# Kernel optimization log

Measured on AMD Instinct MI355X. Metric: run time of the kernel, lower is better.

## Reference

```python
import jax, jax.numpy as jnp
import numpy as np

EMBED_DIM = 1024
NUM_HEADS = 16
RANK = 32
HEAD_DIM = EMBED_DIM // NUM_HEADS
SCALE = 1.0 / np.sqrt(RANK).astype(np.float32)


def setup_inputs() -> dict:
    key = jax.random.key(0)
    ks = jax.random.split(key, 9)
    B, S = 2, 2048
    def lin(k, fan_in, fan_out):
        bound = 1.0 / np.sqrt(fan_in)
        return jax.random.uniform(k, (fan_in, fan_out), jnp.float32, -bound, bound)
    return {
        "hidden_states": jax.random.normal(ks[0], (B, S, EMBED_DIM), jnp.float32),
        "Wq": lin(ks[1], EMBED_DIM, RANK * NUM_HEADS),
        "bq": jnp.zeros((RANK * NUM_HEADS,), jnp.float32),
        "Wk": lin(ks[2], EMBED_DIM, RANK * NUM_HEADS),
        "bk": jnp.zeros((RANK * NUM_HEADS,), jnp.float32),
        "Wv": lin(ks[3], EMBED_DIM, EMBED_DIM),
        "bv": jnp.zeros((EMBED_DIM,), jnp.float32),
        "Wo": lin(ks[4], EMBED_DIM, EMBED_DIM),
        "bo": jnp.zeros((EMBED_DIM,), jnp.float32),
    }


def reference(hidden_states, Wq, bq, Wk, bk, Wv, bv, Wo, bo):
    B, S, E = hidden_states.shape
    q = (hidden_states @ Wq + bq).reshape(B, S, NUM_HEADS, RANK)      # [b,i,h,r]
    k = (hidden_states @ Wk + bk).reshape(B, S, NUM_HEADS, RANK)      # [b,j,h,r]
    v = (hidden_states @ Wv + bv).reshape(B, S, NUM_HEADS, HEAD_DIM)  # [b,j,h,d]
    # full [b,i,j,h] score tensor, softmax over j (axis=2), as in the torch code
    scores = jnp.einsum('bihr,bjhr->bijh', q, k) * SCALE
    attn = jax.nn.softmax(scores, axis=2)
    out = jnp.einsum('bijh,bjhd->bihd', attn, v).reshape(B, S, E)
    return out @ Wo + bo
```

## Files before the change

### kernel.cpp

```cpp
#include <hip/hip_runtime.h>

#define EMBED   1024
#define NHEADS  16
#define RANK    32
#define HDIM    64
#define BATCH   2
#define SEQ     2048
#define BSQ     (BATCH * SEQ)
#define CEXP    0.25505998f

typedef __attribute__((ext_vector_type(8))) short bf16x8;
typedef __attribute__((ext_vector_type(4))) float f32x4;

__device__ __forceinline__ float bf2f(unsigned short u) {
    union { unsigned int i; float f; } x; x.i = ((unsigned int)u) << 16;
    return x.f;
}
__device__ __forceinline__ unsigned short f2bf(float f) {
    union { float f; unsigned int i; } x; x.f = f;
    unsigned int r = x.i + 0x7FFFu + ((x.i >> 16) & 1u);
    return (unsigned short)(r >> 16);
}

#define ASYNC16(gp, lp) \
    __builtin_amdgcn_global_load_lds( \
        (const __attribute__((address_space(1))) void*)(gp), \
        (__attribute__((address_space(3))) void*)(lp), 16, 0, 0)

__global__ __launch_bounds__(256) void prep_all(
    const float* __restrict__ hs,
    const float* __restrict__ Wq, const float* __restrict__ Wk,
    const float* __restrict__ Wv, const float* __restrict__ Wo,
    const float* __restrict__ bq, const float* __restrict__ bk,
    const float* __restrict__ bv,
    unsigned short* __restrict__ hsb, unsigned short* __restrict__ wT_all,
    unsigned short* __restrict__ woT, float* __restrict__ ball)
{
    __shared__ float L[64][65];
    const int blk = blockIdx.x;
    const int t = threadIdx.x;

    if (blk < 2048) {
        const size_t i = ((size_t)blk * 256 + t) * 8;
        float4 v0 = *(const float4*)(hs + i);
        float4 v1 = *(const float4*)(hs + i + 4);
        ushort4 o0, o1;
        o0.x = f2bf(v0.x); o0.y = f2bf(v0.y); o0.z = f2bf(v0.z); o0.w = f2bf(v0.w);
        o1.x = f2bf(v1.x); o1.y = f2bf(v1.y); o1.z = f2bf(v1.z); o1.w = f2bf(v1.w);
        *(ushort4*)(hsb + i) = o0;
        *(ushort4*)(hsb + i + 4) = o1;
        return;
    }
    if (blk < 2816) {
        int idx = blk - 2048;
        int z, bx, by;
        if (idx < 256) { z = idx >> 7; int r2 = idx & 127; bx = r2 & 7; by = r2 >> 3; }
        else { idx -= 256; z = 2 + (idx >> 8); int r2 = idx & 255; bx = r2 & 15; by = r2 >> 4; }
        const int Nw = (z < 2) ? 512 : 1024;
        const float* W = (z == 0) ? Wq : (z == 1) ? Wk : (z == 2) ? Wv : Wo;
        unsigned short* dst = (z == 3) ? woT : (wT_all + (size_t)z * 512 * 1024);

        const int r = t >> 2, c0 = (t & 3) * 16;
        const float* src = W + (size_t)(by * 64 + r) * Nw + bx * 64 + c0;
        #pragma unroll
        for (int u = 0; u < 4; u++)
            *(float4*)&L[r][c0 + 4 * u] = *(const float4*)(src + 4 * u);
        __syncthreads();
        unsigned short* drow = dst + (size_t)(bx * 64 + r) * 1024 + by * 64 + c0;
        #pragma unroll
        for (int u4 = 0; u4 < 4; u4++) {
            ushort4 o;
            o.x = f2bf(L[c0 + 4 * u4 + 0][r]);
            o.y = f2bf(L[c0 + 4 * u4 + 1][r]);
            o.z = f2bf(L[c0 + 4 * u4 + 2][r]);
            o.w = f2bf(L[c0 + 4 * u4 + 3][r]);
            *(ushort4*)(drow + 4 * u4) = o;
        }
        return;
    }
    {
        const int i = (blk - 2816) * 256 + t;
        ball[i] = (i < 512) ? bq[i] : (i < 1024) ? bk[i - 512] : bv[i - 1024];
    }
}

__global__ __launch_bounds__(256) void gemm_qkv(
    const unsigned short* __restrict__ A, const unsigned short* __restrict__ BT,
    const float* __restrict__ bias,
    unsigned short* __restrict__ qH, unsigned short* __restrict__ kH,
    unsigned short* __restrict__ vTout)
{
    __shared__ unsigned short As[2 * 128 * 32];
    __shared__ unsigned short Bs[2 * 128 * 32];
    const int K = 1024;
    const int t = threadIdx.x;
    const int lane = t & 63;
    const int li = lane & 15, la = lane >> 4;
    const int w = t >> 6, wm = w >> 1, wn = w & 1;
    const int row0 = blockIdx.y * 128, col0 = blockIdx.x * 128;

    const int sr = lane >> 2, sc2 = (lane & 3) * 8;
    const unsigned short* ag = A + (size_t)(row0 + sr) * K + sc2;
    const unsigned short* bg = BT + (size_t)(col0 + sr) * K + sc2;

    f32x4 acc[4][4];
    #pragma unroll
    for (int i = 0; i < 4; i++)
        #pragma unroll
        for (int j = 0; j < 4; j++)
            acc[i][j] = (f32x4){0.f, 0.f, 0.f, 0.f};

    for (int k0 = 0; k0 < K; k0 += 64) {
        #pragma unroll
        for (int kh = 0; kh < 2; kh++)
            #pragma unroll
            for (int u = 0; u < 2; u++) {
                const int ro = w * 32 + u * 16;
                ASYNC16(ag + (size_t)ro * K + k0 + kh * 32, &As[kh * 4096 + ro * 32]);
                ASYNC16(bg + (size_t)ro * K + k0 + kh * 32, &Bs[kh * 4096 + ro * 32]);
            }
        __syncthreads();
        #pragma unroll
        for (int kh = 0; kh < 2; kh++) {
            bf16x8 af[4], bfr[4];
            #pragma unroll
            for (int mt = 0; mt < 4; mt++)
                af[mt] = *(const bf16x8*)&As[kh * 4096 + (wm * 64 + mt * 16 + li) * 32 + la * 8];
            #pragma unroll
            for (int nt = 0; nt < 4; nt++)
                bfr[nt] = *(const bf16x8*)&Bs[kh * 4096 + (wn * 64 + nt * 16 + li) * 32 + la * 8];
            #pragma unroll
            for (int mt = 0; mt < 4; mt++)
                #pragma unroll
                for (int nt = 0; nt < 4; nt++)
                    acc[mt][nt] = __builtin_amdgcn_mfma_f32_16x16x32_bf16(af[mt], bfr[nt], acc[mt][nt], 0, 0, 0);
        }
        __syncthreads();
    }

    const int bb = row0 >> 11;
    const int jb = (row0 & 2047) + wm * 64;
    #pragma unroll
    for (int nt = 0; nt < 4; nt++) {
        const int col = col0 + wn * 64 + nt * 16 + li;
        const float bval = bias[col];
        if (col < 1024) {
            const int hh = (col & 511) >> 5;
            const int rr = col & 31;
            unsigned short* base = ((col < 512) ? qH : kH)
                + ((size_t)(bb * 16 + hh) * 2048) * 32 + rr;
            #pragma unroll
            for (int mt = 0; mt < 4; mt++)
                #pragma unroll
                for (int r = 0; r < 4; r++)
                    base[(size_t)(jb + mt * 16 + la * 4 + r) * 32] =
                        f2bf(acc[mt][nt][r] + bval);
        } else {
            const int hd = col - 1024;
            unsigned short* dcol = vTout + ((size_t)(bb * 16 + (hd >> 6)) * 64 + (hd & 63)) * SEQ;
            #pragma unroll
            for (int mt = 0; mt < 4; mt++) {
                const int srow = jb + mt * 16 + la * 4;
                ushort4 o;
                o.x = f2bf(acc[mt][nt][0] + bval);
                o.y = f2bf(acc[mt][nt][1] + bval);
                o.z = f2bf(acc[mt][nt][2] + bval);
                o.w = f2bf(acc[mt][nt][3] + bval);
                *(ushort4*)(dcol + srow) = o;
            }
        }
    }
}

__global__ __launch_bounds__(256) void gemm_out(
    const unsigned short* __restrict__ A, const unsigned short* __restrict__ BT,
    const float* __restrict__ bias, float* __restrict__ C)
{
    __shared__ unsigned short As[2 * 64 * 32];
    __shared__ unsigned short Bs[2 * 128 * 32];
    const int K = 1024;
    const int t = threadIdx.x;
    const int lane = t & 63;
    const int li = lane & 15, la = lane >> 4;
    const int w = t >> 6, wm = w >> 1, wn = w & 1;
    const int row0 = blockIdx.y * 64, col0 = blockIdx.x * 128;

    const int sr = lane >> 2, sc2 = (lane & 3) * 8;
    const unsigned short* ag = A + (size_t)(row0 + sr) * K + sc2;
    const unsigned short* bg = BT + (size_t)(col0 + sr) * K + sc2;

    f32x4 acc[2][4];
    #pragma unroll
    for (int i = 0; i < 2; i++)
        #pragma unroll
        for (int j = 0; j < 4; j++)
            acc[i][j] = (f32x4){0.f, 0.f, 0.f, 0.f};

    for (int k0 = 0; k0 < K; k0 += 64) {
        #pragma unroll
        for (int kh = 0; kh < 2; kh++) {
            ASYNC16(ag + (size_t)(w * 16) * K + k0 + kh * 32, &As[kh * 2048 + (w * 16) * 32]);
            #pragma unroll
            for (int u = 0; u < 2; u++) {
                const int ro = w * 32 + u * 16;
                ASYNC16(bg + (size_t)ro * K + k0 + kh * 32, &Bs[kh * 4096 + ro * 32]);
            }
        }
        __syncthreads();
        #pragma unroll
        for (int kh = 0; kh < 2; kh++) {
            bf16x8 af[2], bfr[4];
            #pragma unroll
            for (int mt = 0; mt < 2; mt++)
                af[mt] = *(const bf16x8*)&As[kh * 2048 + (wm * 32 + mt * 16 + li) * 32 + la * 8];
            #pragma unroll
            for (int nt = 0; nt < 4; nt++)
                bfr[nt] = *(const bf16x8*)&Bs[kh * 4096 + (wn * 64 + nt * 16 + li) * 32 + la * 8];
            #pragma unroll
            for (int mt = 0; mt < 2; mt++)
                #pragma unroll
                for (int nt = 0; nt < 4; nt++)
                    acc[mt][nt] = __builtin_amdgcn_mfma_f32_16x16x32_bf16(af[mt], bfr[nt], acc[mt][nt], 0, 0, 0);
        }
        __syncthreads();
    }

    #pragma unroll
    for (int nt = 0; nt < 4; nt++) {
        const int col = col0 + wn * 64 + nt * 16 + li;
        const float bval = bias[col];
        #pragma unroll
        for (int mt = 0; mt < 2; mt++)
            #pragma unroll
            for (int r = 0; r < 4; r++) {
                const int row = row0 + wm * 32 + mt * 16 + la * 4 + r;
                C[(size_t)row * 1024 + col] = acc[mt][nt][r] + bval;
            }
    }
}

__global__ __launch_bounds__(256) void attn_v8(
    const unsigned short* __restrict__ qH,
    const unsigned short* __restrict__ kH,
    const unsigned short* __restrict__ vT,
    unsigned short* __restrict__ ao)
{
    __shared__ unsigned short kt[2][64 * 48];
    __shared__ unsigned short vt[2][64 * 72];
    __shared__ unsigned short P[64 * 72];

    const int t = threadIdx.x;
    const int lane = t & 63;
    const int li = lane & 15, la = lane >> 4;
    const int w = t >> 6;

    const int bh = blockIdx.x & 31;
    const int itile = blockIdx.x >> 5;
    const int i0 = itile * 64;
    const int b = bh >> 4, h = bh & 15;

    bf16x8 qf;
    {
        const unsigned short* qp = qH + ((size_t)bh * 2048 + i0 + w * 16 + li) * 32 + la * 8;
        ushort4 q0 = *(const ushort4*)qp;
        ushort4 q1 = *(const ushort4*)(qp + 4);
        short u[8];
        u[0] = (short)f2bf(bf2f(q0.x) * CEXP);
        u[1] = (short)f2bf(bf2f(q0.y) * CEXP);
        u[2] = (short)f2bf(bf2f(q0.z) * CEXP);
        u[3] = (short)f2bf(bf2f(q0.w) * CEXP);
        u[4] = (short)f2bf(bf2f(q1.x) * CEXP);
        u[5] = (short)f2bf(bf2f(q1.y) * CEXP);
        u[6] = (short)f2bf(bf2f(q1.z) * CEXP);
        u[7] = (short)f2bf(bf2f(q1.w) * CEXP);
        qf = *(const bf16x8*)u;
    }

    bf16x8 vones;
    #pragma unroll
    for (int u2 = 0; u2 < 8; u2++) vones[u2] = (short)0x3F80;

    const int kr = t >> 2, kc = (t & 3) * 8;
    const int vr = t >> 3, vc = (t & 7) * 8;
    const unsigned short* kp = kH + (size_t)bh * 2048 * 32 + (size_t)kr * 32 + kc;
    const unsigned short* vp0 = vT + (size_t)bh * 64 * SEQ + (size_t)vr * SEQ + vc;
    const unsigned short* vp1 = vp0 + (size_t)32 * SEQ;

    f32x4 accO[4], accl;
    accl = (f32x4){0.f, 0.f, 0.f, 0.f};
    #pragma unroll
    for (int dt = 0; dt < 4; dt++) accO[dt] = (f32x4){0.f, 0.f, 0.f, 0.f};
    const int prow = w * 16 + li;

    uint4 kreg  = *(const uint4*)(kp);
    uint4 vreg0 = *(const uint4*)(vp0);
    uint4 vreg1 = *(const uint4*)(vp1);
    *(uint4*)&kt[0][kr * 48 + kc] = kreg;
    *(uint4*)&vt[0][vr * 72 + vc] = vreg0;
    *(uint4*)&vt[0][(vr + 32) * 72 + vc] = vreg1;
    kreg  = *(const uint4*)(kp + 64 * 32);
    vreg0 = *(const uint4*)(vp0 + 64);
    vreg1 = *(const uint4*)(vp1 + 64);

    #define ATTN_BODY(BUF, OTHER, JPRE)                                            \
    {                                                                              \
        __syncthreads();                                                           \
        *(uint4*)&kt[OTHER][kr * 48 + kc] = kreg;                                  \
        *(uint4*)&vt[OTHER][vr * 72 + vc] = vreg0;                                 \
        *(uint4*)&vt[OTHER][(vr + 32) * 72 + vc] = vreg1;                          \
        const int jn = (JPRE) & 2047;                                              \
        kreg  = *(const uint4*)(kp + (size_t)jn * 32);                             \
        vreg0 = *(const uint4*)(vp0 + jn);                                         \
        vreg1 = *(const uint4*)(vp1 + jn);                                         \
        f32x4 sc[4];                                                               \
        _Pragma("unroll")                                                          \
        for (int jt = 0; jt < 4; jt++) {                                           \
            const bf16x8 kf = *(const bf16x8*)&kt[BUF][(jt * 16 + li) * 48 + la * 8]; \
            sc[jt] = __builtin_amdgcn_mfma_f32_16x16x32_bf16(kf, qf, (f32x4){0.f,0.f,0.f,0.f}, 0, 0, 0); \
        }                                                                          \
        _Pragma("unroll")                                                          \
        for (int jt = 0; jt < 4; jt++) {                                           \
            union { float f; unsigned int u; } c0, c1, c2, c3;                     \
            c0.f = exp2f(sc[jt][0]);                                               \
            c1.f = exp2f(sc[jt][1]);                                               \
            c2.f = exp2f(sc[jt][2]);                                               \
            c3.f = exp2f(sc[jt][3]);                                               \
            uint2 pk;                                                              \
            pk.x = __builtin_amdgcn_perm(c1.u + 0x8000u, c0.u + 0x8000u, 0x07060302u); \
            pk.y = __builtin_amdgcn_perm(c3.u + 0x8000u, c2.u + 0x8000u, 0x07060302u); \
            *(uint2*)&P[prow * 72 + jt * 16 + la * 4] = pk;                        \
        }                                                                          \
        _Pragma("unroll")                                                          \
        for (int ks = 0; ks < 2; ks++) {                                           \
            const bf16x8 pf = *(const bf16x8*)&P[prow * 72 + ks * 32 + la * 8];    \
            accl = __builtin_amdgcn_mfma_f32_16x16x32_bf16(pf, vones, accl, 0, 0, 0); \
            _Pragma("unroll")                                                      \
            for (int dt = 0; dt < 4; dt++) {                                       \
                const bf16x8 vf = *(const bf16x8*)&vt[BUF][(dt * 16 + li) * 72 + ks * 32 + la * 8]; \
                accO[dt] = __builtin_amdgcn_mfma_f32_16x16x32_bf16(pf, vf, accO[dt], 0, 0, 0); \
            }                                                                      \
        }                                                                          \
    }

    for (int j0 = 0; j0 < SEQ; j0 += 128) {
        ATTN_BODY(0, 1, j0 + 128)
        ATTN_BODY(1, 0, j0 + 192)
    }
    #undef ATTN_BODY

    float linv[4];
    #pragma unroll
    for (int r = 0; r < 4; r++) linv[r] = 1.f / accl[r];
    #pragma unroll
    for (int dt = 0; dt < 4; dt++)
        #pragma unroll
        for (int r = 0; r < 4; r++) {
            const int row = b * SEQ + i0 + w * 16 + la * 4 + r;
            ao[(size_t)row * 1024 + h * 64 + dt * 16 + li] = f2bf(accO[dt][r] * linv[r]);
        }
}

extern "C" void kernel_launch(void* const* d_in, const int* in_sizes, int n_in,
                              void* d_out, int out_size, void* d_ws, size_t ws_size,
                              hipStream_t stream) {
    const float* hs = (const float*)d_in[0];
    const float* Wq = (const float*)d_in[1];
    const float* bq = (const float*)d_in[2];
    const float* Wk = (const float*)d_in[3];
    const float* bk = (const float*)d_in[4];
    const float* Wv = (const float*)d_in[5];
    const float* bv = (const float*)d_in[6];
    const float* Wo = (const float*)d_in[7];
    const float* bo = (const float*)d_in[8];

    char* p = (char*)d_ws;
    unsigned short* hsb = (unsigned short*)(p);
    unsigned short* wT  = (unsigned short*)(p + 8388608u);
    unsigned short* woT = (unsigned short*)(p + 12582912u);
    float*          ball= (float*)(p + 14680064u);
    unsigned short* qHb = (unsigned short*)(p + 14688256u);
    unsigned short* kHb = (unsigned short*)(p + 18882560u);
    unsigned short* vTb = (unsigned short*)(p + 23076864u);
    unsigned short* ao  = (unsigned short*)(p + 31465472u);

    prep_all<<<dim3(2824), 256, 0, stream>>>(hs, Wq, Wk, Wv, Wo, bq, bk, bv,
                                             hsb, wT, woT, ball);

    gemm_qkv<<<dim3(16, 32), 256, 0, stream>>>(hsb, wT, ball, qHb, kHb, vTb);

    attn_v8<<<dim3(1024), 256, 0, stream>>>(qHb, kHb, vTb, ao);

    gemm_out<<<dim3(8, 64), 256, 0, stream>>>(ao, woT, bo, (float*)d_out);
}
```

Measured before the change: 189.5 us.

## Double-buffer LDS tiles in QKV/out GEMMs and simplify attention prefetch addressing

The QKV and output projection GEMMs now use two LDS buffers, so the next K-tile is loaded asynchronously while MFMAs run on the current one. This is meant to hide global-load latency that the single-buffer version exposed before every compute step. The cost is double the shared memory per block, which may lower occupancy. The attention kernel's K/V prefetch now uses incrementing pointers instead of wrapped index math. That removes the wrap, so the final iterations read past the end of each head's slice; the data is never used, but the read may go past the buffer end for the last head.

Measured after the change: 196.4 us. +3.7%, slower.

```diff
diff --git a/kernel.cpp b/kernel.cpp
--- a/kernel.cpp
+++ b/kernel.cpp
@@ -90,8 +90,8 @@
     unsigned short* __restrict__ qH, unsigned short* __restrict__ kH,
     unsigned short* __restrict__ vTout)
 {
-    __shared__ unsigned short As[2 * 128 * 32];
-    __shared__ unsigned short Bs[2 * 128 * 32];
+    __shared__ unsigned short As[2][128 * 64];
+    __shared__ unsigned short Bs[2][128 * 64];
     const int K = 1024;
     const int t = threadIdx.x;
     const int lane = t & 63;
@@ -103,6 +103,18 @@
     const unsigned short* ag = A + (size_t)(row0 + sr) * K + sc2;
     const unsigned short* bg = BT + (size_t)(col0 + sr) * K + sc2;
 
+#define STAGE_QKV(BUF, KOFF)                                                     \
+    {                                                                            \
+        _Pragma("unroll")                                                        \
+        for (int kh = 0; kh < 2; kh++)                                           \
+            _Pragma("unroll")                                                    \
+            for (int u = 0; u < 2; u++) {                                        \
+                const int ro = w * 32 + u * 16;                                  \
+                ASYNC16(ag + (size_t)ro * K + (KOFF) + kh * 32, &As[BUF][kh * 4096 + ro * 32]); \
+                ASYNC16(bg + (size_t)ro * K + (KOFF) + kh * 32, &Bs[BUF][kh * 4096 + ro * 32]); \
+            }                                                                    \
+    }
+
     f32x4 acc[4][4];
     #pragma unroll
     for (int i = 0; i < 4; i++)
@@ -110,25 +122,21 @@
         for (int j = 0; j < 4; j++)
             acc[i][j] = (f32x4){0.f, 0.f, 0.f, 0.f};
 
+    STAGE_QKV(0, 0)
+    __syncthreads();
+
     for (int k0 = 0; k0 < K; k0 += 64) {
-        #pragma unroll
-        for (int kh = 0; kh < 2; kh++)
-            #pragma unroll
-            for (int u = 0; u < 2; u++) {
-                const int ro = w * 32 + u * 16;
-                ASYNC16(ag + (size_t)ro * K + k0 + kh * 32, &As[kh * 4096 + ro * 32]);
-                ASYNC16(bg + (size_t)ro * K + k0 + kh * 32, &Bs[kh * 4096 + ro * 32]);
-            }
-        __syncthreads();
+        const int cur = (k0 >> 6) & 1;
+        if (k0 + 64 < K) STAGE_QKV(cur ^ 1, k0 + 64)
         #pragma unroll
         for (int kh = 0; kh < 2; kh++) {
             bf16x8 af[4], bfr[4];
             #pragma unroll
             for (int mt = 0; mt < 4; mt++)
-                af[mt] = *(const bf16x8*)&As[kh * 4096 + (wm * 64 + mt * 16 + li) * 32 + la * 8];
+                af[mt] = *(const bf16x8*)&As[cur][kh * 4096 + (wm * 64 + mt * 16 + li) * 32 + la * 8];
             #pragma unroll
             for (int nt = 0; nt < 4; nt++)
-                bfr[nt] = *(const bf16x8*)&Bs[kh * 4096 + (wn * 64 + nt * 16 + li) * 32 + la * 8];
+                bfr[nt] = *(const bf16x8*)&Bs[cur][kh * 4096 + (wn * 64 + nt * 16 + li) * 32 + la * 8];
             #pragma unroll
             for (int mt = 0; mt < 4; mt++)
                 #pragma unroll
@@ -137,6 +145,7 @@
         }
         __syncthreads();
     }
+#undef STAGE_QKV
 
     const int bb = row0 >> 11;
     const int jb = (row0 & 2047) + wm * 64;
@@ -176,8 +185,8 @@
     const unsigned short* __restrict__ A, const unsigned short* __restrict__ BT,
     const float* __restrict__ bias, float* __restrict__ C)
 {
-    __shared__ unsigned short As[2 * 64 * 32];
-    __shared__ unsigned short Bs[2 * 128 * 32];
+    __shared__ unsigned short As[2][64 * 64];
+    __shared__ unsigned short Bs[2][128 * 64];
     const int K = 1024;
     const int t = threadIdx.x;
     const int lane = t & 63;
@@ -189,6 +198,19 @@
     const unsigned short* ag = A + (size_t)(row0 + sr) * K + sc2;
     const unsigned short* bg = BT + (size_t)(col0 + sr) * K + sc2;
 
+#define STAGE_OUT(BUF, KOFF)                                                     \
+    {                                                                            \
+        _Pragma("unroll")                                                        \
+        for (int kh = 0; kh < 2; kh++) {                                         \
+            ASYNC16(ag + (size_t)(w * 16) * K + (KOFF) + kh * 32, &As[BUF][kh * 2048 + (w * 16) * 32]); \
+            _Pragma("unroll")                                                    \
+            for (int u = 0; u < 2; u++) {                                        \
+                const int ro = w * 32 + u * 16;                                  \
+                ASYNC16(bg + (size_t)ro * K + (KOFF) + kh * 32, &Bs[BUF][kh * 4096 + ro * 32]); \
+            }                                                                    \
+        }                                                                        \
+    }
+
     f32x4 acc[2][4];
     #pragma unroll
     for (int i = 0; i < 2; i++)
@@ -196,26 +218,21 @@
         for (int j = 0; j < 4; j++)
             acc[i][j] = (f32x4){0.f, 0.f, 0.f, 0.f};
 
+    STAGE_OUT(0, 0)
+    __syncthreads();
+
     for (int k0 = 0; k0 < K; k0 += 64) {
-        #pragma unroll
-        for (int kh = 0; kh < 2; kh++) {
-            ASYNC16(ag + (size_t)(w * 16) * K + k0 + kh * 32, &As[kh * 2048 + (w * 16) * 32]);
-            #pragma unroll
-            for (int u = 0; u < 2; u++) {
-                const int ro = w * 32 + u * 16;
-                ASYNC16(bg + (size_t)ro * K + k0 + kh * 32, &Bs[kh * 4096 + ro * 32]);
-            }
-        }
-        __syncthreads();
+        const int cur = (k0 >> 6) & 1;
+        if (k0 + 64 < K) STAGE_OUT(cur ^ 1, k0 + 64)
         #pragma unroll
         for (int kh = 0; kh < 2; kh++) {
             bf16x8 af[2], bfr[4];
             #pragma unroll
             for (int mt = 0; mt < 2; mt++)
-                af[mt] = *(const bf16x8*)&As[kh * 2048 + (wm * 32 + mt * 16 + li) * 32 + la * 8];
+                af[mt] = *(const bf16x8*)&As[cur][kh * 2048 + (wm * 32 + mt * 16 + li) * 32 + la * 8];
             #pragma unroll
             for (int nt = 0; nt < 4; nt++)
-                bfr[nt] = *(const bf16x8*)&Bs[kh * 4096 + (wn * 64 + nt * 16 + li) * 32 + la * 8];
+                bfr[nt] = *(const bf16x8*)&Bs[cur][kh * 4096 + (wn * 64 + nt * 16 + li) * 32 + la * 8];
             #pragma unroll
             for (int mt = 0; mt < 2; mt++)
                 #pragma unroll
@@ -224,6 +241,7 @@
         }
         __syncthreads();
     }
+#undef STAGE_OUT
 
     #pragma unroll
     for (int nt = 0; nt < 4; nt++) {
@@ -301,17 +319,19 @@
     kreg  = *(const uint4*)(kp + 64 * 32);
     vreg0 = *(const uint4*)(vp0 + 64);
     vreg1 = *(const uint4*)(vp1 + 64);
-
-    #define ATTN_BODY(BUF, OTHER, JPRE)                                            \
+    const unsigned short* kpf  = kp + 2 * 64 * 32;
+    const unsigned short* vpf0 = vp0 + 128;
+    const unsigned short* vpf1 = vp1 + 128;
+
+    #define ATTN_BODY(BUF, OTHER, KOFF, VOFF)                                      \
     {                                                                              \
         __syncthreads();                                                           \
         *(uint4*)&kt[OTHER][kr * 48 + kc] = kreg;                                  \
         *(uint4*)&vt[OTHER][vr * 72 + vc] = vreg0;                                 \
         *(uint4*)&vt[OTHER][(vr + 32) * 72 + vc] = vreg1;                          \
-        const int jn = (JPRE) & 2047;                                              \
-        kreg  = *(const uint4*)(kp + (size_t)jn * 32);                             \
-        vreg0 = *(const uint4*)(vp0 + jn);                                         \
-        vreg1 = *(const uint4*)(vp1 + jn);                                         \
+        kreg  = *(const uint4*)(kpf + (KOFF));                                     \
+        vreg0 = *(const uint4*)(vpf0 + (VOFF));                                    \
+        vreg1 = *(const uint4*)(vpf1 + (VOFF));                                    \
         f32x4 sc[4];                                                               \
         _Pragma("unroll")                                                          \
         for (int jt = 0; jt < 4; jt++) {                                           \
@@ -343,8 +363,11 @@
     }
 
     for (int j0 = 0; j0 < SEQ; j0 += 128) {
-        ATTN_BODY(0, 1, j0 + 128)
-        ATTN_BODY(1, 0, j0 + 192)
+        ATTN_BODY(0, 1, 0, 0)
+        ATTN_BODY(1, 0, 64 * 32, 64)
+        kpf  += 128 * 32;
+        vpf0 += 128;
+        vpf1 += 128;
     }
     #undef ATTN_BODY
 
```

## Process 128 query rows per attention block to reuse K/V tiles

Applied to the files above, without the earlier changes.

Each attention block now covers 128 query rows instead of 64, and each wave handles two 16-row query tiles. Every K/V tile staged in shared memory therefore serves twice as many score and PV MFMAs, which halves global K/V traffic and barrier count per query row. Prefetch addressing moves to incrementing pointers and drops the wrap-around mask, so the last iterations read past the per-head slice into adjacent workspace (the data is unused). The trade-offs are half as many blocks (512), more registers per thread from the doubled accumulators, and a larger P buffer in shared memory, all of which can lower occupancy.

Measured after the change: 190.1 us. Within noise of the previous version (+0.3%).

```diff
diff --git a/kernel.cpp b/kernel.cpp
--- a/kernel.cpp
+++ b/kernel.cpp
@@ -239,7 +239,7 @@
     }
 }
 
-__global__ __launch_bounds__(256) void attn_v8(
+__global__ __launch_bounds__(256) void attn_v7(
     const unsigned short* __restrict__ qH,
     const unsigned short* __restrict__ kH,
     const unsigned short* __restrict__ vT,
@@ -247,7 +247,7 @@
 {
     __shared__ unsigned short kt[2][64 * 48];
     __shared__ unsigned short vt[2][64 * 72];
-    __shared__ unsigned short P[64 * 72];
+    __shared__ unsigned short P[128 * 72];
 
     const int t = threadIdx.x;
     const int lane = t & 63;
@@ -256,12 +256,13 @@
 
     const int bh = blockIdx.x & 31;
     const int itile = blockIdx.x >> 5;
-    const int i0 = itile * 64;
+    const int i0 = itile * 128;
     const int b = bh >> 4, h = bh & 15;
 
-    bf16x8 qf;
-    {
-        const unsigned short* qp = qH + ((size_t)bh * 2048 + i0 + w * 16 + li) * 32 + la * 8;
+    bf16x8 qf[2];
+    #pragma unroll
+    for (int it = 0; it < 2; it++) {
+        const unsigned short* qp = qH + ((size_t)bh * 2048 + i0 + w * 32 + it * 16 + li) * 32 + la * 8;
         ushort4 q0 = *(const ushort4*)qp;
         ushort4 q1 = *(const ushort4*)(qp + 4);
         short u[8];
@@ -273,7 +274,7 @@
         u[5] = (short)f2bf(bf2f(q1.y) * CEXP);
         u[6] = (short)f2bf(bf2f(q1.z) * CEXP);
         u[7] = (short)f2bf(bf2f(q1.w) * CEXP);
-        qf = *(const bf16x8*)u;
+        qf[it] = *(const bf16x8*)u;
     }
 
     bf16x8 vones;
@@ -286,11 +287,13 @@
     const unsigned short* vp0 = vT + (size_t)bh * 64 * SEQ + (size_t)vr * SEQ + vc;
     const unsigned short* vp1 = vp0 + (size_t)32 * SEQ;
 
-    f32x4 accO[4], accl;
-    accl = (f32x4){0.f, 0.f, 0.f, 0.f};
-    #pragma unroll
-    for (int dt = 0; dt < 4; dt++) accO[dt] = (f32x4){0.f, 0.f, 0.f, 0.f};
-    const int prow = w * 16 + li;
+    f32x4 accO[2][4], accl[2];
+    #pragma unroll
+    for (int mt = 0; mt < 2; mt++) {
+        accl[mt] = (f32x4){0.f, 0.f, 0.f, 0.f};
+        #pragma unroll
+        for (int dt = 0; dt < 4; dt++) accO[mt][dt] = (f32x4){0.f, 0.f, 0.f, 0.f};
+    }
 
     uint4 kreg  = *(const uint4*)(kp);
     uint4 vreg0 = *(const uint4*)(vp0);
@@ -301,63 +304,77 @@
     kreg  = *(const uint4*)(kp + 64 * 32);
     vreg0 = *(const uint4*)(vp0 + 64);
     vreg1 = *(const uint4*)(vp1 + 64);
-
-    #define ATTN_BODY(BUF, OTHER, JPRE)                                            \
+    const unsigned short* kpf  = kp + 2 * 64 * 32;
+    const unsigned short* vpf0 = vp0 + 128;
+    const unsigned short* vpf1 = vp1 + 128;
+
+    #define ATTN_BODY(BUF, OTHER, KOFF, VOFF)                                      \
     {                                                                              \
         __syncthreads();                                                           \
         *(uint4*)&kt[OTHER][kr * 48 + kc] = kreg;                                  \
         *(uint4*)&vt[OTHER][vr * 72 + vc] = vreg0;                                 \
         *(uint4*)&vt[OTHER][(vr + 32) * 72 + vc] = vreg1;                          \
-        const int jn = (JPRE) & 2047;                                              \
-        kreg  = *(const uint4*)(kp + (size_t)jn * 32);                             \
-        vreg0 = *(const uint4*)(vp0 + jn);                                         \
-        vreg1 = *(const uint4*)(vp1 + jn);                                         \
-        f32x4 sc[4];                                                               \
+        kreg  = *(const uint4*)(kpf + (KOFF));                                     \
+        vreg0 = *(const uint4*)(vpf0 + (VOFF));                                    \
+        vreg1 = *(const uint4*)(vpf1 + (VOFF));                                    \
+        f32x4 sc[4][2];                                                            \
         _Pragma("unroll")                                                          \
         for (int jt = 0; jt < 4; jt++) {                                           \
             const bf16x8 kf = *(const bf16x8*)&kt[BUF][(jt * 16 + li) * 48 + la * 8]; \
-            sc[jt] = __builtin_amdgcn_mfma_f32_16x16x32_bf16(kf, qf, (f32x4){0.f,0.f,0.f,0.f}, 0, 0, 0); \
+            sc[jt][0] = __builtin_amdgcn_mfma_f32_16x16x32_bf16(kf, qf[0], (f32x4){0.f,0.f,0.f,0.f}, 0, 0, 0); \
+            sc[jt][1] = __builtin_amdgcn_mfma_f32_16x16x32_bf16(kf, qf[1], (f32x4){0.f,0.f,0.f,0.f}, 0, 0, 0); \
         }                                                                          \
         _Pragma("unroll")                                                          \
-        for (int jt = 0; jt < 4; jt++) {                                           \
-            union { float f; unsigned int u; } c0, c1, c2, c3;                     \
-            c0.f = exp2f(sc[jt][0]);                                               \
-            c1.f = exp2f(sc[jt][1]);                                               \
-            c2.f = exp2f(sc[jt][2]);                                               \
-            c3.f = exp2f(sc[jt][3]);                                               \
-            uint2 pk;                                                              \
-            pk.x = __builtin_amdgcn_perm(c1.u + 0x8000u, c0.u + 0x8000u, 0x07060302u); \
-            pk.y = __builtin_amdgcn_perm(c3.u + 0x8000u, c2.u + 0x8000u, 0x07060302u); \
-            *(uint2*)&P[prow * 72 + jt * 16 + la * 4] = pk;                        \
-        }                                                                          \
+        for (int jt = 0; jt < 4; jt++)                                             \
+            _Pragma("unroll")                                                      \
+            for (int it = 0; it < 2; it++) {                                       \
+                union { float f; unsigned int u; } c0, c1, c2, c3;                 \
+                c0.f = exp2f(sc[jt][it][0]);                                       \
+                c1.f = exp2f(sc[jt][it][1]);                                       \
+                c2.f = exp2f(sc[jt][it][2]);                                       \
+                c3.f = exp2f(sc[jt][it][3]);                                       \
+                uint2 pk;                                                          \
+                pk.x = __builtin_amdgcn_perm(c1.u + 0x8000u, c0.u + 0x8000u, 0x07060302u); \
+                pk.y = __builtin_amdgcn_perm(c3.u + 0x8000u, c2.u + 0x8000u, 0x07060302u); \
+                *(uint2*)&P[(w * 32 + it * 16 + li) * 72 + jt * 16 + la * 4] = pk; \
+            }                                                                      \
         _Pragma("unroll")                                                          \
-        for (int ks = 0; ks < 2; ks++) {                                           \
-            const bf16x8 pf = *(const bf16x8*)&P[prow * 72 + ks * 32 + la * 8];    \
-            accl = __builtin_amdgcn_mfma_f32_16x16x32_bf16(pf, vones, accl, 0, 0, 0); \
+        for (int mt = 0; mt < 2; mt++) {                                           \
             _Pragma("unroll")                                                      \
-            for (int dt = 0; dt < 4; dt++) {                                       \
-                const bf16x8 vf = *(const bf16x8*)&vt[BUF][(dt * 16 + li) * 72 + ks * 32 + la * 8]; \
-                accO[dt] = __builtin_amdgcn_mfma_f32_16x16x32_bf16(pf, vf, accO[dt], 0, 0, 0); \
+            for (int ks = 0; ks < 2; ks++) {                                       \
+                const bf16x8 pf = *(const bf16x8*)&P[(w * 32 + mt * 16 + li) * 72 + ks * 32 + la * 8]; \
+                accl[mt] = __builtin_amdgcn_mfma_f32_16x16x32_bf16(pf, vones, accl[mt], 0, 0, 0); \
+                _Pragma("unroll")                                                  \
+                for (int dt = 0; dt < 4; dt++) {                                   \
+                    const bf16x8 vf = *(const bf16x8*)&vt[BUF][(dt * 16 + li) * 72 + ks * 32 + la * 8]; \
+                    accO[mt][dt] = __builtin_amdgcn_mfma_f32_16x16x32_bf16(pf, vf, accO[mt][dt], 0, 0, 0); \
+                }                                                                  \
             }                                                                      \
         }                                                                          \
     }
 
     for (int j0 = 0; j0 < SEQ; j0 += 128) {
-        ATTN_BODY(0, 1, j0 + 128)
-        ATTN_BODY(1, 0, j0 + 192)
+        ATTN_BODY(0, 1, 0, 0)
+        ATTN_BODY(1, 0, 64 * 32, 64)
+        kpf  += 128 * 32;
+        vpf0 += 128;
+        vpf1 += 128;
     }
     #undef ATTN_BODY
 
-    float linv[4];
-    #pragma unroll
-    for (int r = 0; r < 4; r++) linv[r] = 1.f / accl[r];
-    #pragma unroll
-    for (int dt = 0; dt < 4; dt++)
-        #pragma unroll
-        for (int r = 0; r < 4; r++) {
-            const int row = b * SEQ + i0 + w * 16 + la * 4 + r;
-            ao[(size_t)row * 1024 + h * 64 + dt * 16 + li] = f2bf(accO[dt][r] * linv[r]);
-        }
+    #pragma unroll
+    for (int mt = 0; mt < 2; mt++) {
+        float linv[4];
+        #pragma unroll
+        for (int r = 0; r < 4; r++) linv[r] = 1.f / accl[mt][r];
+        #pragma unroll
+        for (int dt = 0; dt < 4; dt++)
+            #pragma unroll
+            for (int r = 0; r < 4; r++) {
+                const int row = b * SEQ + i0 + w * 32 + mt * 16 + la * 4 + r;
+                ao[(size_t)row * 1024 + h * 64 + dt * 16 + li] = f2bf(accO[mt][dt][r] * linv[r]);
+            }
+    }
 }
 
 extern "C" void kernel_launch(void* const* d_in, const int* in_sizes, int n_in,
@@ -388,7 +405,7 @@
 
     gemm_qkv<<<dim3(16, 32), 256, 0, stream>>>(hsb, wT, ball, qHb, kHb, vTb);
 
-    attn_v8<<<dim3(1024), 256, 0, stream>>>(qHb, kHb, vTb, ao);
+    attn_v7<<<dim3(512), 256, 0, stream>>>(qHb, kHb, vTb, ao);
 
     gemm_out<<<dim3(8, 64), 256, 0, stream>>>(ao, woT, bo, (float*)d_out);
 }
```
